# Kernel optimization log

Hardware: AMD Instinct MI355X
Metric: run time of the kernel (lower is better)

The kernel has to match this reference:

```python
import jax, jax.numpy as jnp
import numpy as np

B, T, D, H = 4, 1024, 1024, 16
DS, DC, EXP = 16, 4, 2
DI = EXP * D            # 2048 inner SSM dim
DTR = D // 16           # 64 dt rank
K = max(1, int(0.2 * T))  # top-k tokens routed to attention
HD = D // H


def setup_inputs() -> dict:
    key = jax.random.key(0)
    ks = jax.random.split(key, 12)
    s = 0.02
    w = lambda k, shp: jax.random.normal(k, shp, jnp.float32) * s
    return {
        "x": jax.random.normal(ks[0], (B, T, D), jnp.float32),
        "ln_gamma": jnp.ones((D,), jnp.float32),
        "ln_beta": jnp.zeros((D,), jnp.float32),
        "Wr1": w(ks[1], (D, D // 4)), "br1": jnp.zeros((D // 4,), jnp.float32),
        "Wr2": w(ks[2], (D // 4, 1)), "br2": jnp.zeros((1,), jnp.float32),
        "Wqkv": w(ks[3], (D, 3 * D)), "bqkv": jnp.zeros((3 * D,), jnp.float32),
        "Wo": w(ks[4], (D, D)), "bo": jnp.zeros((D,), jnp.float32),
        "W_in": w(ks[5], (D, 2 * DI)),
        "conv_w": w(ks[6], (DI, DC)), "conv_b": jnp.zeros((DI,), jnp.float32),
        "W_xproj": w(ks[7], (DI, DTR + 2 * DS)),
        "W_dt": w(ks[8], (DTR, DI)), "b_dt": jnp.zeros((DI,), jnp.float32),
        "A_log": jnp.log(jnp.broadcast_to(jnp.arange(1, DS + 1, dtype=jnp.float32), (DI, DS))),
        "Dskip": jnp.ones((DI,), jnp.float32),
        "W_out": w(ks[9], (DI, D)),
    }


def _layernorm(x, g, b):
    mu = x.mean(-1, keepdims=True)
    v = ((x - mu) ** 2).mean(-1, keepdims=True)
    return (x - mu) * jax.lax.rsqrt(v + 1e-5) * g + b


def _attn(tok, Wqkv, bqkv, Wo, bo):
    # full MHA over the k selected tokens only: tok (B,K,D)
    qkv = tok @ Wqkv + bqkv
    q, k_, v = jnp.split(qkv, 3, axis=-1)
    q = q.reshape(B, K, H, HD).transpose(0, 2, 1, 3)   # bhkd
    k_ = k_.reshape(B, K, H, HD).transpose(0, 2, 1, 3)
    v = v.reshape(B, K, H, HD).transpose(0, 2, 1, 3)
    scores = jnp.einsum('bhqd,bhkd->bhqk', q, k_) / jnp.sqrt(jnp.float32(HD))
    p = jax.nn.softmax(scores, axis=-1)
    o = jnp.einsum('bhqk,bhkd->bhqd', p, v)
    o = o.transpose(0, 2, 1, 3).reshape(B, K, D)
    return o @ Wo + bo


def _ssm(xn, W_in, conv_w, conv_b, W_xproj, W_dt, b_dt, A_log, Dskip, W_out):
    # Mamba-style selective SSM over all tokens
    u, z = jnp.split(xn @ W_in, 2, axis=-1)            # (B,T,DI) each
    up = jnp.pad(u, ((0, 0), (DC - 1, 0), (0, 0)))      # causal depthwise conv
    uc = sum(up[:, j:j + T, :] * conv_w[:, j] for j in range(DC)) + conv_b
    u = jax.nn.silu(uc)
    proj = u @ W_xproj                                  # (B,T,DTR+2*DS)
    dt = jax.nn.softplus(proj[..., :DTR] @ W_dt + b_dt)  # (B,T,DI)
    Bm = proj[..., DTR:DTR + DS]                        # (B,T,DS)
    Cm = proj[..., DTR + DS:]                           # (B,T,DS)
    A = -jnp.exp(A_log)                                 # (DI,DS)
    dA = jnp.exp(dt[..., None] * A)                     # (B,T,DI,DS)
    dBu = dt[..., None] * Bm[:, :, None, :] * u[..., None]

    def step(h, inp):
        dA_t, dBu_t, C_t = inp
        h = dA_t * h + dBu_t                            # (B,DI,DS)
        y = (h * C_t[:, None, :]).sum(-1)               # (B,DI)
        return h, y

    h0 = jnp.zeros((B, DI, DS), dA.dtype)
    _, ys = jax.lax.scan(step, h0, (dA.transpose(1, 0, 2, 3),
                                    dBu.transpose(1, 0, 2, 3),
                                    Cm.transpose(1, 0, 2)))
    y = ys.transpose(1, 0, 2) + u * Dskip               # (B,T,DI)
    y = y * jax.nn.silu(z)
    return y @ W_out


def reference(x, ln_gamma, ln_beta, Wr1, br1, Wr2, br2, Wqkv, bqkv, Wo, bo,
              W_in, conv_w, conv_b, W_xproj, W_dt, b_dt, A_log, Dskip, W_out):
    xn = _layernorm(x, ln_gamma, ln_beta)
    scores = (jax.nn.relu(xn @ Wr1 + br1) @ Wr2 + br2)[..., 0]   # (B,T)
    _, idx = jax.lax.top_k(scores, K)                            # (B,K)
    bidx = jnp.arange(B)[:, None]
    mask = jnp.zeros((B, T), bool).at[bidx, idx].set(True)
    delta_ssm = _ssm(xn, W_in, conv_w, conv_b, W_xproj, W_dt, b_dt, A_log, Dskip, W_out)
    tok = xn[bidx, idx]                                          # gather (B,K,D)
    delta_tok = _attn(tok, Wqkv, bqkv, Wo, bo)
    delta_attn = jnp.zeros_like(xn).at[bidx, idx].set(delta_tok)  # scatter back
    delta = jnp.where(mask[..., None], delta_attn, delta_ssm)
    return x + delta
```

## Files before the change

### kernel.cpp

```cpp
#include <hip/hip_runtime.h>
#include <hip/hip_bf16.h>
#include <math.h>

#define BB   4
#define TT   1024
#define DD   1024
#define HH   16
#define DII  2048
#define DSS  16
#define DCC  4
#define KK   204
#define HDD  64
#define DTRR 64
#define NCH  32
#define LCH  32
#define KSPL 8
#define XPN  96
#define PRJ  128
#define RZ   8
#define RKC  3072

typedef short bf16x8 __attribute__((ext_vector_type(8)));
typedef short bf16x4v __attribute__((ext_vector_type(4)));
typedef float f32x4 __attribute__((ext_vector_type(4)));

#define GLDS16(g, l) __builtin_amdgcn_global_load_lds(                        \
    (const __attribute__((address_space(1))) void*)(g),                       \
    (__attribute__((address_space(3))) void*)(l), 16, 0, 0)

__device__ __forceinline__ ushort f2bu(float v) {
  __hip_bfloat16 h = __float2bfloat16(v);
  return __builtin_bit_cast(ushort, h);
}
__device__ __forceinline__ float b2f(ushort u) {
  __hip_bfloat16 h = __builtin_bit_cast(__hip_bfloat16, u);
  return __bfloat162float(h);
}

__device__ __forceinline__ float wave_sum(float v) {
#pragma unroll
  for (int o = 32; o > 0; o >>= 1) v += __shfl_xor(v, o, 64);
  return v;
}
__device__ __forceinline__ float block_sum256(float v, volatile float* sh) {
  v = wave_sum(v);
  if ((threadIdx.x & 63) == 0) sh[threadIdx.x >> 6] = v;
  __syncthreads();
  float r = sh[0] + sh[1] + sh[2] + sh[3];
  __syncthreads();
  return r;
}

__global__ __launch_bounds__(256) void layernorm_kernel(
    const float* __restrict__ x, const float* __restrict__ g,
    const float* __restrict__ be, ushort* __restrict__ xcat) {
  __shared__ float sh[4];
  int row = blockIdx.x;
  const float* xr = x + (size_t)row * DD;
  float v[4];
  float s = 0.f;
#pragma unroll
  for (int i = 0; i < 4; i++) { v[i] = xr[threadIdx.x + 256 * i]; s += v[i]; }
  float mean = block_sum256(s, sh) * (1.f / DD);
  float q = 0.f;
#pragma unroll
  for (int i = 0; i < 4; i++) { float d = v[i] - mean; q += d * d; }
  float var = block_sum256(q, sh) * (1.f / DD);
  float rstd = rsqrtf(var + 1e-5f);
  ushort* xc = xcat + (size_t)row * RKC;
#pragma unroll
  for (int i = 0; i < 4; i++) {
    int c = threadIdx.x + 256 * i;
    float o = (v[i] - mean) * rstd * g[c] + be[c];
    ushort hi = f2bu(o);
    float lo = o - b2f(hi);
    xc[c] = hi;
    xc[1024 + c] = hi;
    xc[2048 + c] = f2bu(lo);
  }
}

__device__ __forceinline__ void tile_transpose(
    const float* W, int rows, int cols, ushort* WT, int bx, int by,
    float tile[32][33]) {
  int c0 = bx * 32, r0 = by * 32;
  int tx = threadIdx.x & 31, ty = threadIdx.x >> 5;
#pragma unroll
  for (int i = 0; i < 32; i += 8)
    tile[ty + i][tx] = W[(size_t)(r0 + ty + i) * cols + c0 + tx];
  __syncthreads();
#pragma unroll
  for (int i = 0; i < 32; i += 8)
    WT[(size_t)(c0 + ty + i) * rows + r0 + tx] = f2bu(tile[tx][ty + i]);
}

__global__ __launch_bounds__(256) void transpose_all(
    const float* __restrict__ W_in, const float* __restrict__ W_out,
    const float* __restrict__ Wqkv, const float* __restrict__ Wo,
    const float* __restrict__ W_dt, const float* __restrict__ W_xproj,
    ushort* __restrict__ WinT, ushort* __restrict__ WoutT,
    ushort* __restrict__ WqkvT, ushort* __restrict__ WoT,
    ushort* __restrict__ WdtT, ushort* __restrict__ WxprojT) {
  __shared__ float tile[32][33];
  int lin = blockIdx.x;
  if (lin < 4096) {
    tile_transpose(W_in, 1024, 4096, WinT, lin % 128, lin / 128, tile);
  } else if ((lin -= 4096) < 2048) {
    tile_transpose(W_out, 2048, 1024, WoutT, lin % 32, lin / 32, tile);
  } else if ((lin -= 2048) < 3072) {
    tile_transpose(Wqkv, 1024, 3072, WqkvT, lin % 96, lin / 96, tile);
  } else if ((lin -= 3072) < 1024) {
    tile_transpose(Wo, 1024, 1024, WoT, lin % 32, lin / 32, tile);
  } else if ((lin -= 1024) < 128) {
    tile_transpose(W_dt, 64, 2048, WdtT, lin % 64, lin / 64, tile);
  } else {
    lin -= 128;
    tile_transpose(W_xproj, 2048, 96, WxprojT, lin % 3, lin / 3, tile);
  }
}

__global__ __launch_bounds__(256) void transpose_hilo(
    const float* __restrict__ W, ushort* __restrict__ WT) {
  __shared__ float tile[32][33];
  int c0 = blockIdx.x * 32, r0 = blockIdx.y * 32;
  int tx = threadIdx.x & 31, ty = threadIdx.x >> 5;
#pragma unroll
  for (int i = 0; i < 32; i += 8)
    tile[ty + i][tx] = W[(size_t)(r0 + ty + i) * 256 + c0 + tx];
  __syncthreads();
#pragma unroll
  for (int i = 0; i < 32; i += 8) {
    float v = tile[tx][ty + i];
    ushort hi = f2bu(v);
    float lo = v - b2f(hi);
    size_t base = (size_t)(c0 + ty + i) * RKC;
    WT[base + r0 + tx] = hi;
    WT[base + 1024 + r0 + tx] = f2bu(lo);
    WT[base + 2048 + r0 + tx] = hi;
  }
}

__global__ __launch_bounds__(512) void gemm_bf16_256(
    const ushort* __restrict__ A, int lda,
    const ushort* __restrict__ BT, int ldbt,
    void* __restrict__ Cv, int ldc, int K,
    const float* __restrict__ bias, const float* __restrict__ addmat,
    int outBf16) {
  __shared__ ushort Alds[256 * 64];
  __shared__ ushort Blds[256 * 64];
  int t = threadIdx.x;
  int wv = t >> 6, lane = t & 63;
  int wvm = wv >> 2, wvn = wv & 3;
  int nwg = gridDim.x * gridDim.y;
  int lin = blockIdx.y * gridDim.x + blockIdx.x;
  int swz = (lin & 7) * (nwg >> 3) + (lin >> 3);
  int bx = swz % gridDim.x, by = swz / gridDim.x;
  int row0 = by * 256, col0 = bx * 256;
  f32x4 acc[8][4] = {};

  const ushort* Ap[4];
  const ushort* Bp[4];
  ushort* Alb[4];
  ushort* Blb[4];
#pragma unroll
  for (int j = 0; j < 4; j++) {
    int c = j * 512 + t;
    int r = c >> 3;
    int kc = (((c & 7) ^ (r & 7)) * 8);
    Ap[j] = A + (size_t)(row0 + r) * lda + kc;
    Bp[j] = BT + (size_t)(col0 + r) * ldbt + kc;
    int cst = j * 512 + wv * 64;
    Alb[j] = Alds + (size_t)cst * 8;
    Blb[j] = Blds + (size_t)cst * 8;
  }
  int frow = lane & 15, fk = (lane >> 4) * 8;

  for (int k0 = 0; k0 < K; k0 += 64) {
#pragma unroll
    for (int j = 0; j < 4; j++) {
      GLDS16(Ap[j] + k0, Alb[j]);
      GLDS16(Bp[j] + k0, Blb[j]);
    }
    __syncthreads();
#pragma unroll
    for (int ks = 0; ks < 2; ks++) {
      bf16x8 af[8], bfv[4];
#pragma unroll
      for (int m = 0; m < 8; m++) {
        int row = wvm * 128 + m * 16 + frow;
        af[m] = *(const bf16x8*)&Alds[row * 64 +
                                      ((ks * 32 + fk) ^ ((row & 7) * 8))];
      }
#pragma unroll
      for (int n = 0; n < 4; n++) {
        int row = wvn * 64 + n * 16 + frow;
        bfv[n] = *(const bf16x8*)&Blds[row * 64 +
                                       ((ks * 32 + fk) ^ ((row & 7) * 8))];
      }
#pragma unroll
      for (int m = 0; m < 8; m++)
#pragma unroll
        for (int n = 0; n < 4; n++)
          acc[m][n] = __builtin_amdgcn_mfma_f32_16x16x32_bf16(af[m], bfv[n],
                                                              acc[m][n], 0, 0, 0);
    }
    __syncthreads();
  }
  int rbase = row0 + wvm * 128 + (lane >> 4) * 4;
  int cbase = col0 + wvn * 64 + (lane & 15);
  if (outBf16) {
    ushort* myL = Alds + wv * 1088;
    ushort* C16 = (ushort*)Cv;
    for (int m = 0; m < 8; m++) {
      __syncthreads();
#pragma unroll
      for (int n = 0; n < 4; n++) {
        int cc = cbase + n * 16;
        float bi = bias ? bias[cc] : 0.f;
#pragma unroll
        for (int i = 0; i < 4; i++)
          myL[((lane >> 4) * 4 + i) * 68 + (lane & 15) + n * 16] =
              f2bu(acc[m][n][i] + bi);
      }
      __syncthreads();
      int rr = lane >> 2, cg = lane & 3;
      bf16x8 v0 = *(const bf16x8*)&myL[rr * 68 + cg * 16];
      bf16x8 v1 = *(const bf16x8*)&myL[rr * 68 + cg * 16 + 8];
      size_t grow = (size_t)(row0 + wvm * 128 + m * 16 + rr) * ldc +
                    col0 + wvn * 64 + cg * 16;
      *(bf16x8*)&C16[grow] = v0;
      *(bf16x8*)&C16[grow + 8] = v1;
    }
  } else {
    float* C = (float*)Cv;
#pragma unroll
    for (int n = 0; n < 4; n++) {
      int cc = cbase + n * 16;
      float bi = bias ? bias[cc] : 0.f;
#pragma unroll
      for (int m = 0; m < 8; m++) {
#pragma unroll
        for (int i = 0; i < 4; i++) {
          size_t r = rbase + m * 16 + i;
          float v = acc[m][n][i] + bi;
          if (addmat) v += addmat[r * ldc + cc];
          C[r * ldc + cc] = v;
        }
      }
    }
  }
}

__global__ __launch_bounds__(512) void gemm_bf16_128x8(
    const ushort* __restrict__ A, int lda,
    const ushort* __restrict__ BT, int ldbt,
    void* __restrict__ Cv, int ldc, int K,
    const float* __restrict__ bias, const float* __restrict__ addmat,
    int act, int outBf16) {
  __shared__ ushort Alds[128 * 64];
  __shared__ ushort Blds[128 * 64];
  int t = threadIdx.x;
  int wv = t >> 6, lane = t & 63;
  int wvm = wv >> 1, wvn = wv & 1;
  int nwg = gridDim.x * gridDim.y;
  int lin = blockIdx.y * gridDim.x + blockIdx.x;
  int swz = (lin & 7) * (nwg >> 3) + (lin >> 3);
  int bx = swz % gridDim.x, by = swz / gridDim.x;
  int row0 = by * 128, col0 = bx * 128;
  f32x4 acc[2][4] = {};

  const ushort* Ap[2];
  const ushort* Bp[2];
  ushort* Alb[2];
  ushort* Blb[2];
#pragma unroll
  for (int j = 0; j < 2; j++) {
    int c = j * 512 + t;
    int r = c >> 3;
    int kc = (((c & 7) ^ (r & 7)) * 8);
    Ap[j] = A + (size_t)(row0 + r) * lda + kc;
    Bp[j] = BT + (size_t)(col0 + r) * ldbt + kc;
    int cst = j * 512 + wv * 64;
    Alb[j] = Alds + (size_t)cst * 8;
    Blb[j] = Blds + (size_t)cst * 8;
  }
  int frow = lane & 15, fk = (lane >> 4) * 8;

  for (int k0 = 0; k0 < K; k0 += 64) {
#pragma unroll
    for (int j = 0; j < 2; j++) {
      GLDS16(Ap[j] + k0, Alb[j]);
      GLDS16(Bp[j] + k0, Blb[j]);
    }
    __syncthreads();
#pragma unroll
    for (int ks = 0; ks < 2; ks++) {
      bf16x8 af[2], bfv[4];
#pragma unroll
      for (int m = 0; m < 2; m++) {
        int row = wvm * 32 + m * 16 + frow;
        af[m] = *(const bf16x8*)&Alds[row * 64 +
                                      ((ks * 32 + fk) ^ ((row & 7) * 8))];
      }
#pragma unroll
      for (int n = 0; n < 4; n++) {
        int row = wvn * 64 + n * 16 + frow;
        bfv[n] = *(const bf16x8*)&Blds[row * 64 +
                                       ((ks * 32 + fk) ^ ((row & 7) * 8))];
      }
#pragma unroll
      for (int m = 0; m < 2; m++)
#pragma unroll
        for (int n = 0; n < 4; n++)
          acc[m][n] = __builtin_amdgcn_mfma_f32_16x16x32_bf16(af[m], bfv[n],
                                                              acc[m][n], 0, 0, 0);
    }
    __syncthreads();
  }
  int rbase = row0 + wvm * 32 + (lane >> 4) * 4;
  int cbase = col0 + wvn * 64 + (lane & 15);
#pragma unroll
  for (int n = 0; n < 4; n++) {
    int cc = cbase + n * 16;
    float bi = bias ? bias[cc] : 0.f;
#pragma unroll
    for (int m = 0; m < 2; m++) {
#pragma unroll
      for (int i = 0; i < 4; i++) {
        size_t r = rbase + m * 16 + i;
        float v = acc[m][n][i] + bi;
        if (act == 2) v = (v > 20.f) ? v : log1pf(__expf(v));
        if (outBf16) {
          ((ushort*)Cv)[r * ldc + cc] = f2bu(v);
        } else {
          if (addmat) v += addmat[r * ldc + cc];
          ((float*)Cv)[r * ldc + cc] = v;
        }
      }
    }
  }
}

__global__ __launch_bounds__(512) void gemm_bf16_128x8_splitk(
    const ushort* __restrict__ A, int lda,
    const ushort* __restrict__ BT, int ldbt,
    float* __restrict__ partial, int ldc, int Ktot, size_t zstride) {
  __shared__ ushort Alds[128 * 64];
  __shared__ ushort Blds[128 * 64];
  int t = threadIdx.x;
  int wv = t >> 6, lane = t & 63;
  int wvm = wv >> 1, wvn = wv & 1;
  int nwg = gridDim.x * gridDim.y;
  int lin = blockIdx.y * gridDim.x + blockIdx.x;
  int swz = (lin & 7) * (nwg >> 3) + (lin >> 3);
  int bx = swz % gridDim.x, by = swz / gridDim.x;
  int row0 = by * 128, col0 = bx * 128;
  int kchunk = Ktot / gridDim.z;
  int kbeg = blockIdx.z * kchunk, kend = kbeg + kchunk;
  f32x4 acc[2][4] = {};

  const ushort* Ap[2];
  const ushort* Bp[2];
  ushort* Alb[2];
  ushort* Blb[2];
#pragma unroll
  for (int j = 0; j < 2; j++) {
    int c = j * 512 + t;
    int r = c >> 3;
    int kc = (((c & 7) ^ (r & 7)) * 8);
    Ap[j] = A + (size_t)(row0 + r) * lda + kc;
    Bp[j] = BT + (size_t)(col0 + r) * ldbt + kc;
    int cst = j * 512 + wv * 64;
    Alb[j] = Alds + (size_t)cst * 8;
    Blb[j] = Blds + (size_t)cst * 8;
  }
  int frow = lane & 15, fk = (lane >> 4) * 8;

  for (int k0 = kbeg; k0 < kend; k0 += 64) {
#pragma unroll
    for (int j = 0; j < 2; j++) {
      GLDS16(Ap[j] + k0, Alb[j]);
      GLDS16(Bp[j] + k0, Blb[j]);
    }
    __syncthreads();
#pragma unroll
    for (int ks = 0; ks < 2; ks++) {
      bf16x8 af[2], bfv[4];
#pragma unroll
      for (int m = 0; m < 2; m++) {
        int row = wvm * 32 + m * 16 + frow;
        af[m] = *(const bf16x8*)&Alds[row * 64 +
                                      ((ks * 32 + fk) ^ ((row & 7) * 8))];
      }
#pragma unroll
      for (int n = 0; n < 4; n++) {
        int row = wvn * 64 + n * 16 + frow;
        bfv[n] = *(const bf16x8*)&Blds[row * 64 +
                                       ((ks * 32 + fk) ^ ((row & 7) * 8))];
      }
#pragma unroll
      for (int m = 0; m < 2; m++)
#pragma unroll
        for (int n = 0; n < 4; n++)
          acc[m][n] = __builtin_amdgcn_mfma_f32_16x16x32_bf16(af[m], bfv[n],
                                                              acc[m][n], 0, 0, 0);
    }
    __syncthreads();
  }
  float* P = partial + (size_t)blockIdx.z * zstride;
  int rbase = row0 + wvm * 32 + (lane >> 4) * 4;
  int cbase = col0 + wvn * 64 + (lane & 15);
#pragma unroll
  for (int n = 0; n < 4; n++) {
    int cc = cbase + n * 16;
#pragma unroll
    for (int m = 0; m < 2; m++)
#pragma unroll
      for (int i = 0; i < 4; i++)
        P[(size_t)(rbase + m * 16 + i) * ldc + cc] = acc[m][n][i];
  }
}

__global__ __launch_bounds__(256) void router_score_reduce(
    const float* __restrict__ rpart, const float* __restrict__ br1,
    const float* __restrict__ Wr2, const float* __restrict__ br2,
    float* __restrict__ scores, size_t zstride) {
  __shared__ float sh[4];
  int row = blockIdx.x, c = threadIdx.x;
  size_t idx = (size_t)row * 256 + c;
  float s = 0.f;
#pragma unroll
  for (int z = 0; z < RZ; z++) s += rpart[z * zstride + idx];
  s = fmaxf(s + br1[c], 0.f);
  float tot = block_sum256(s * Wr2[c], sh);
  if (c == 0) scores[row] = tot + br2[0];
}

__global__ __launch_bounds__(256) void gemm_bf16_mfma(
    const ushort* __restrict__ A, int lda,
    const ushort* __restrict__ BT, int ldbt,
    float* __restrict__ C, int ldc,
    int M, int N, int K, const float* __restrict__ bias,
    const float* __restrict__ addmat, const int* __restrict__ rowmap) {
  __shared__ ushort Alds[128 * 32];
  __shared__ ushort Blds[128 * 32];
  int t = threadIdx.x;
  int wv = t >> 6;
  int lane = t & 63;
  int nwg = gridDim.x * gridDim.y;
  int lin = blockIdx.y * gridDim.x + blockIdx.x;
  int swz = (lin & 7) * (nwg >> 3) + (lin >> 3);
  int bx = swz % gridDim.x, by = swz / gridDim.x;
  int row0 = by * 128, col0 = bx * 128;
  int wr = (wv >> 1) * 64, wc = (wv & 1) * 64;
  f32x4 acc[4][4] = {};

  int srow = t >> 2;
  int sk = (((t & 3) ^ (srow & 3)) * 8);
  int ar0 = row0 + srow;       if (ar0 >= M) ar0 = M - 1;
  int ar1 = row0 + 64 + srow;  if (ar1 >= M) ar1 = M - 1;
  int br0 = col0 + srow;       if (br0 >= N) br0 = N - 1;
  int br1 = col0 + 64 + srow;  if (br1 >= N) br1 = N - 1;
  const ushort* Ag0 = A + (size_t)ar0 * lda + sk;
  const ushort* Ag1 = A + (size_t)ar1 * lda + sk;
  const ushort* Bg0 = BT + (size_t)br0 * ldbt + sk;
  const ushort* Bg1 = BT + (size_t)br1 * ldbt + sk;
  ushort* Al = Alds + wv * 512;
  ushort* Bl = Blds + wv * 512;

  int frow = lane & 15;
  int fk = (lane >> 4) * 8;

  for (int k0 = 0; k0 < K; k0 += 32) {
    GLDS16(Ag0 + k0, Al);
    GLDS16(Ag1 + k0, Al + 2048);
    GLDS16(Bg0 + k0, Bl);
    GLDS16(Bg1 + k0, Bl + 2048);
    __syncthreads();
    bf16x8 af[4], bfv[4];
#pragma unroll
    for (int m = 0; m < 4; m++) {
      int row = wr + m * 16 + frow;
      af[m] = *(const bf16x8*)&Alds[row * 32 + (fk ^ ((row & 3) * 8))];
    }
#pragma unroll
    for (int n = 0; n < 4; n++) {
      int row = wc + n * 16 + frow;
      bfv[n] = *(const bf16x8*)&Blds[row * 32 + (fk ^ ((row & 3) * 8))];
    }
#pragma unroll
    for (int m = 0; m < 4; m++)
#pragma unroll
      for (int n = 0; n < 4; n++)
        acc[m][n] = __builtin_amdgcn_mfma_f32_16x16x32_bf16(af[m], bfv[n],
                                                            acc[m][n], 0, 0, 0);
    __syncthreads();
  }
  int rbase = row0 + wr + (lane >> 4) * 4;
  int cbase = col0 + wc + (lane & 15);
#pragma unroll
  for (int n = 0; n < 4; n++) {
    int ccol = cbase + n * 16;
    if (ccol >= N) continue;
    float bi = bias ? bias[ccol] : 0.f;
#pragma unroll
    for (int m = 0; m < 4; m++) {
      int r0_ = rbase + m * 16;
#pragma unroll
      for (int i = 0; i < 4; i++) {
        int r = r0_ + i;
        if (r < M) {
          size_t orow = r;
          if (rowmap) orow = (size_t)((r / KK) * TT + rowmap[r]);
          float v = acc[m][n][i] + bi;
          if (addmat) v += addmat[orow * ldc + ccol];
          C[orow * ldc + ccol] = v;
        }
      }
    }
  }
}

__global__ __launch_bounds__(1024) void topk_kernel(
    const float* __restrict__ scores, int* __restrict__ idx) {
  __shared__ float s[1024];
  __shared__ int si[1024];
  int b = blockIdx.x, t = threadIdx.x;
  s[t] = scores[b * TT + t];
  si[t] = t;
  __syncthreads();
  for (int k = 2; k <= 1024; k <<= 1) {
    for (int j = k >> 1; j > 0; j >>= 1) {
      int partner = t ^ j;
      if (partner > t) {
        bool dirDesc = ((t & k) == 0);
        float s1 = s[t], s2 = s[partner];
        int i1 = si[t], i2 = si[partner];
        bool firstGreater = (s1 > s2) || (s1 == s2 && i1 < i2);
        bool doSwap = dirDesc ? !firstGreater : firstGreater;
        if (doSwap) { s[t] = s2; s[partner] = s1; si[t] = i2; si[partner] = i1; }
      }
      __syncthreads();
    }
  }
  if (t < KK) idx[b * KK + t] = si[t];
}

__global__ __launch_bounds__(256) void splitk_reduce_dual(
    const float* __restrict__ partial, float* __restrict__ C,
    __hip_bfloat16* __restrict__ Cb, int MN) {
  int i = blockIdx.x * 256 + threadIdx.x;
  if (i >= MN) return;
  float s = 0.f;
#pragma unroll
  for (int k = 0; k < KSPL; k++) s += partial[(size_t)k * MN + i];
  C[i] = s;
  Cb[i] = __float2bfloat16(s);
}

__global__ __launch_bounds__(256) void conv_silu_kernel(
    const ushort* __restrict__ uz, const float* __restrict__ conv_w,
    const float* __restrict__ conv_b, ushort* __restrict__ ub16) {
  size_t gid4 = ((size_t)blockIdx.x * 256 + threadIdx.x) * 4;
  int c = gid4 % DII;
  size_t bt = gid4 / DII;
  int t = bt % TT;
  int b = bt / TT;
  f32x4 cw[4];
#pragma unroll
  for (int ci = 0; ci < 4; ci++) cw[ci] = *(const f32x4*)&conv_w[(c + ci) * DCC];
  f32x4 sum = *(const f32x4*)&conv_b[c];
#pragma unroll
  for (int j = 0; j < DCC; j++) {
    int tt = t - (DCC - 1) + j;
    if (tt >= 0) {
      bf16x4v uv = *(const bf16x4v*)&uz[((size_t)(b * TT + tt)) * (2 * DII) + c];
#pragma unroll
      for (int ci = 0; ci < 4; ci++) sum[ci] += b2f((ushort)uv[ci]) * cw[ci][j];
    }
  }
  bf16x4v rb;
#pragma unroll
  for (int ci = 0; ci < 4; ci++)
    rb[ci] = (short)f2bu(sum[ci] / (1.f + __expf(-sum[ci])));
  *(bf16x4v*)&ub16[gid4] = rb;
}

__global__ __launch_bounds__(256) void ssm_phase1(
    const ushort* __restrict__ dt, const float* __restrict__ proj,
    const ushort* __restrict__ u, const float* __restrict__ A_log,
    float* __restrict__ hloc, float* __restrict__ Pprod) {
  int gid = blockIdx.x * 256 + threadIdx.x;
  int half = gid & 1;
  int cc = gid >> 1;
  int di = cc % DII;
  int rem = cc / DII;
  int chunk = rem % NCH;
  int b = rem / NCH;
  float a[8], h[8], P[8];
#pragma unroll
  for (int i = 0; i < 2; i++) {
    f32x4 al = *(const f32x4*)&A_log[di * DSS + half * 8 + i * 4];
#pragma unroll
    for (int j = 0; j < 4; j++) a[i * 4 + j] = -__expf(al[j]);
  }
#pragma unroll
  for (int s = 0; s < 8; s++) { h[s] = 0.f; P[s] = 1.f; }
  int t0 = chunk * LCH;
  for (int lt = 0; lt < LCH; lt++) {
    size_t bt = (size_t)(b * TT + t0 + lt);
    float dtv = b2f(dt[bt * DII + di]);
    float uv = b2f(u[bt * DII + di]);
    const float* pr = proj + bt * PRJ + DTRR + half * 8;
    float dtu = dtv * uv;
#pragma unroll
    for (int s = 0; s < 8; s++) {
      float dA = __expf(dtv * a[s]);
      h[s] = dA * h[s] + dtu * pr[s];
      P[s] *= dA;
    }
  }
#pragma unroll
  for (int i = 0; i < 2; i++) {
    *(f32x4*)&hloc[(size_t)cc * 16 + half * 8 + i * 4] = *(f32x4*)&h[i * 4];
    *(f32x4*)&Pprod[(size_t)cc * 16 + half * 8 + i * 4] = *(f32x4*)&P[i * 4];
  }
}

__global__ __launch_bounds__(256) void ssm_phase2(
    const float* __restrict__ hloc, const float* __restrict__ Pprod,
    float* __restrict__ hin) {
  int gid = blockIdx.x * 256 + threadIdx.x;
  int s_di = gid % (DII * 16);
  int b = gid / (DII * 16);
  float run = 0.f;
#pragma unroll
  for (int c = 0; c < NCH; c++) {
    size_t off = ((size_t)(b * NCH + c) * DII) * 16 + s_di;
    hin[off] = run;
    run = Pprod[off] * run + hloc[off];
  }
}

__global__ __launch_bounds__(256) void ssm_phase3(
    const ushort* __restrict__ dt, const float* __restrict__ proj,
    const ushort* __restrict__ u, const ushort* __restrict__ uz,
    const float* __restrict__ A_log, const float* __restrict__ Dskip,
    const float* __restrict__ hin, __hip_bfloat16* __restrict__ y) {
  int gid = blockIdx.x * 256 + threadIdx.x;
  int half = gid & 1;
  int cc = gid >> 1;
  int di = cc % DII;
  int rem = cc / DII;
  int chunk = rem % NCH;
  int b = rem / NCH;
  float a[8], h[8];
#pragma unroll
  for (int i = 0; i < 2; i++) {
    f32x4 al = *(const f32x4*)&A_log[di * DSS + half * 8 + i * 4];
    f32x4 hl = *(const f32x4*)&hin[(size_t)cc * 16 + half * 8 + i * 4];
#pragma unroll
    for (int j = 0; j < 4; j++) { a[i * 4 + j] = -__expf(al[j]); h[i * 4 + j] = hl[j]; }
  }
  float dsk = Dskip[di];
  int t0 = chunk * LCH;
  for (int lt = 0; lt < LCH; lt++) {
    size_t bt = (size_t)(b * TT + t0 + lt);
    float dtv = b2f(dt[bt * DII + di]);
    float uv = b2f(u[bt * DII + di]);
    const float* prB = proj + bt * PRJ + DTRR + half * 8;
    const float* prC = prB + DSS;
    float dtu = dtv * uv;
    float yp = 0.f;
#pragma unroll
    for (int s = 0; s < 8; s++) {
      float dA = __expf(dtv * a[s]);
      h[s] = dA * h[s] + dtu * prB[s];
      yp += h[s] * prC[s];
    }
    yp += __shfl_xor(yp, 1, 64);
    if (half == 0) {
      float zv = b2f(uz[bt * (2 * DII) + DII + di]);
      float sz = zv / (1.f + __expf(-zv));
      y[bt * DII + di] = __float2bfloat16((yp + uv * dsk) * sz);
    }
  }
}

__global__ __launch_bounds__(256) void gather_tok(
    const ushort* __restrict__ xcat, const int* __restrict__ idx,
    ushort* __restrict__ tok) {
  int r = blockIdx.x;
  int b = r / KK;
  int tsel = idx[r];
  const ushort* src = xcat + (size_t)(b * TT + tsel) * RKC;
  ushort* dst = tok + (size_t)r * DD;
#pragma unroll
  for (int j = 0; j < 4; j++) dst[threadIdx.x + 256 * j] = src[threadIdx.x + 256 * j];
}

#define KP 72
#define VP 232
__global__ __launch_bounds__(832) void attn_mfma_kernel(
    const float* __restrict__ qkv, __hip_bfloat16* __restrict__ attn_o) {
  __shared__ ushort Klds[208 * KP];
  __shared__ ushort VTlds[64 * VP];
  __shared__ ushort Plds[13 * 16 * VP];
  int bh = blockIdx.x;
  int h = bh % HH, b = bh / HH;
  int t = threadIdx.x;
  const float* base = qkv + (size_t)(b * KK) * 3072 + h * 64;

  for (int i = t; i < 208 * 64; i += 832) {
    int r = i >> 6, d = i & 63;
    float v = (r < KK) ? base[(size_t)r * 3072 + 1024 + d] : 0.f;
    Klds[r * KP + d] = f2bu(v);
  }
  for (int i = t; i < 208 * 64; i += 832) {
    int r = i >> 6, d = i & 63;
    float v = (r < KK) ? base[(size_t)r * 3072 + 2048 + d] : 0.f;
    VTlds[d * VP + r] = f2bu(v);
  }
  for (int i = t; i < 64 * (VP - 208); i += 832) {
    int d = i / (VP - 208), k = 208 + i % (VP - 208);
    VTlds[d * VP + k] = 0;
  }

  int wv = t >> 6, lane = t & 63;
  int q0 = wv * 16;
  int qrow = q0 + (lane & 15);
  if (qrow > KK - 1) qrow = KK - 1;
  const float* qptr = base + (size_t)qrow * 3072 + ((lane >> 4) * 8);
  bf16x8 qf[2];
#pragma unroll
  for (int ks = 0; ks < 2; ks++) {
    f32x4 lo = *(const f32x4*)(qptr + ks * 32);
    f32x4 hi = *(const f32x4*)(qptr + ks * 32 + 4);
#pragma unroll
    for (int j = 0; j < 4; j++) {
      qf[ks][j] = (short)f2bu(lo[j] * 0.125f);
      qf[ks][j + 4] = (short)f2bu(hi[j] * 0.125f);
    }
  }
  ushort* myP = Plds + wv * 16 * VP;
  for (int i = lane; i < 16 * (VP - 208); i += 64) {
    int r = i / (VP - 208), k = 208 + i % (VP - 208);
    myP[r * VP + k] = 0;
  }
  __syncthreads();

  f32x4 sacc[13] = {};
#pragma unroll
  for (int nt = 0; nt < 13; nt++) {
#pragma unroll
    for (int ks = 0; ks < 2; ks++) {
      bf16x8 kf = *(const bf16x8*)&Klds[(nt * 16 + (lane & 15)) * KP +
                                        ks * 32 + (lane >> 4) * 8];
      sacc[nt] = __builtin_amdgcn_mfma_f32_16x16x32_bf16(qf[ks], kf, sacc[nt], 0, 0, 0);
    }
  }
  if ((lane & 15) >= 12) {
#pragma unroll
    for (int i = 0; i < 4; i++) sacc[12][i] = -1e30f;
  }
  float m4[4], l4[4];
#pragma unroll
  for (int i = 0; i < 4; i++) {
    float m = sacc[0][i];
#pragma unroll
    for (int nt = 1; nt < 13; nt++) m = fmaxf(m, sacc[nt][i]);
    m = fmaxf(m, __shfl_xor(m, 1, 64));
    m = fmaxf(m, __shfl_xor(m, 2, 64));
    m = fmaxf(m, __shfl_xor(m, 4, 64));
    m = fmaxf(m, __shfl_xor(m, 8, 64));
    m4[i] = m;
  }
#pragma unroll
  for (int i = 0; i < 4; i++) {
    float ls = 0.f;
    int prow = (lane >> 4) * 4 + i;
#pragma unroll
    for (int nt = 0; nt < 13; nt++) {
      float e = __expf(sacc[nt][i] - m4[i]);
      ls += e;
      myP[prow * VP + nt * 16 + (lane & 15)] = f2bu(e);
    }
    ls += __shfl_xor(ls, 1, 64);
    ls += __shfl_xor(ls, 2, 64);
    ls += __shfl_xor(ls, 4, 64);
    ls += __shfl_xor(ls, 8, 64);
    l4[i] = ls;
  }
  f32x4 oacc[4] = {};
#pragma unroll
  for (int dt = 0; dt < 4; dt++) {
#pragma unroll
    for (int ks = 0; ks < 7; ks++) {
      bf16x8 pf = *(const bf16x8*)&myP[(lane & 15) * VP + ks * 32 + (lane >> 4) * 8];
      bf16x8 vf = *(const bf16x8*)&VTlds[(dt * 16 + (lane & 15)) * VP +
                                         ks * 32 + (lane >> 4) * 8];
      oacc[dt] = __builtin_amdgcn_mfma_f32_16x16x32_bf16(pf, vf, oacc[dt], 0, 0, 0);
    }
  }
#pragma unroll
  for (int i = 0; i < 4; i++) {
    int row = q0 + (lane >> 4) * 4 + i;
    if (row >= KK) continue;
    float inv = 1.f / l4[i];
#pragma unroll
    for (int dt = 0; dt < 4; dt++) {
      int col = dt * 16 + (lane & 15);
      attn_o[((size_t)(b * KK + row)) * DD + h * 64 + col] =
          __float2bfloat16(oacc[dt][i] * inv);
    }
  }
}

extern "C" void kernel_launch(void* const* d_in, const int* in_sizes, int n_in,
                              void* d_out, int out_size, void* d_ws, size_t ws_size,
                              hipStream_t stream) {
  const float* x = (const float*)d_in[0];
  const float* ln_g = (const float*)d_in[1];
  const float* ln_b = (const float*)d_in[2];
  const float* Wr1 = (const float*)d_in[3];
  const float* br1 = (const float*)d_in[4];
  const float* Wr2 = (const float*)d_in[5];
  const float* br2 = (const float*)d_in[6];
  const float* Wqkv = (const float*)d_in[7];
  const float* bqkv = (const float*)d_in[8];
  const float* Wo = (const float*)d_in[9];
  const float* bo = (const float*)d_in[10];
  const float* W_in = (const float*)d_in[11];
  const float* conv_w = (const float*)d_in[12];
  const float* conv_b = (const float*)d_in[13];
  const float* W_xproj = (const float*)d_in[14];
  const float* W_dt = (const float*)d_in[15];
  const float* b_dt = (const float*)d_in[16];
  const float* A_log = (const float*)d_in[17];
  const float* Dskip = (const float*)d_in[18];
  const float* W_out = (const float*)d_in[19];
  float* out = (float*)d_out;

  float* w = (float*)d_ws;
  size_t o = 0;
  float* scores = w + o; o += (size_t)BB * TT;
  int* idxb = (int*)(w + o); o += 1024;
  ushort* uzb16 = (ushort*)(w + o); o += (size_t)BB * TT * 2 * DII / 2;
  float* projb = w + o;  o += (size_t)BB * TT * PRJ;
  float* qkvb = w + o;   o += (size_t)BB * KK * 3 * DD;
  float* hloc = w + o;   o += (size_t)BB * NCH * DII * 16;
  float* Pprod = w + o;  o += (size_t)BB * NCH * DII * 16;
  float* hin = w + o;    o += (size_t)BB * NCH * DII * 16;
  ushort* xcat = (ushort*)(w + o);                  o += (size_t)BB * TT * RKC / 2;
  __hip_bfloat16* yb16 = (__hip_bfloat16*)(w + o);  o += (size_t)BB * TT * DII / 2;
  ushort* ub16 = (ushort*)(w + o);                  o += (size_t)BB * TT * DII / 2;
  ushort* dtb16 = (ushort*)(w + o);                 o += (size_t)BB * TT * DII / 2;
  ushort* tokb = (ushort*)(w + o);                  o += (size_t)BB * KK * DD / 2 + 8;
  __hip_bfloat16* attno = (__hip_bfloat16*)(w + o); o += (size_t)BB * KK * DD / 2 + 8;
  __hip_bfloat16* projb16 = (__hip_bfloat16*)(w + o); o += (size_t)BB * TT * PRJ / 2 + 8;
  ushort* Wr1cat = (ushort*)(w + o);                o += (size_t)256 * RKC / 2;
  ushort* WinT = (ushort*)(w + o);                  o += (size_t)(2 * DII) * DD / 2;
  ushort* WoutT = (ushort*)(w + o);                 o += (size_t)DD * DII / 2;
  ushort* WqkvT = (ushort*)(w + o);                 o += (size_t)(3 * DD) * DD / 2;
  ushort* WoT = (ushort*)(w + o);                   o += (size_t)DD * DD / 2;
  ushort* WdtT = (ushort*)(w + o);                  o += (size_t)DII * DTRR / 2;
  ushort* WxprojT = (ushort*)(w + o);               o += (size_t)PRJ * DII / 2;
  float* rpart = (float*)uzb16;
  float* xpart = hloc;
  const size_t RZSTR = (size_t)BB * TT * 256;
  const size_t XZSTR = (size_t)BB * TT * PRJ;

  layernorm_kernel<<<BB * TT, 256, 0, stream>>>(x, ln_g, ln_b, xcat);
  transpose_all<<<10560, 256, 0, stream>>>(W_in, W_out, Wqkv, Wo, W_dt, W_xproj,
                                           WinT, WoutT, WqkvT, WoT, WdtT, WxprojT);
  transpose_hilo<<<dim3(256 / 32, DD / 32), 256, 0, stream>>>(Wr1, Wr1cat);
  gemm_bf16_128x8_splitk<<<dim3(256 / 128, BB * TT / 128, RZ), 512, 0, stream>>>(
      xcat, RKC, Wr1cat, RKC, rpart, 256, RKC, RZSTR);
  router_score_reduce<<<BB * TT, 256, 0, stream>>>(rpart, br1, Wr2, br2, scores,
                                                   RZSTR);
  topk_kernel<<<BB, 1024, 0, stream>>>(scores, idxb);
  gemm_bf16_256<<<dim3(2 * DII / 256, BB * TT / 256), 512, 0, stream>>>(
      xcat, RKC, WinT, DD, uzb16, 2 * DII, DD, nullptr, nullptr, 1);
  conv_silu_kernel<<<(BB * TT * DII) / 1024, 256, 0, stream>>>(uzb16, conv_w,
                                                               conv_b, ub16);
  gemm_bf16_128x8_splitk<<<dim3(PRJ / 128, BB * TT / 128, KSPL), 512, 0, stream>>>(
      ub16, DII, WxprojT, DII, xpart, PRJ, DII, XZSTR);
  splitk_reduce_dual<<<(int)((XZSTR + 255) / 256), 256, 0, stream>>>(
      xpart, projb, projb16, (int)XZSTR);
  gemm_bf16_128x8<<<dim3(DII / 128, BB * TT / 128), 512, 0, stream>>>(
      (const ushort*)projb16, PRJ, WdtT, DTRR, dtb16, DII, DTRR,
      b_dt, nullptr, 2, 1);
  ssm_phase1<<<(BB * NCH * DII * 2) / 256, 256, 0, stream>>>(dtb16, projb, ub16,
                                                             A_log, hloc, Pprod);
  ssm_phase2<<<(BB * DII * 16) / 256, 256, 0, stream>>>(hloc, Pprod, hin);
  ssm_phase3<<<(BB * NCH * DII * 2) / 256, 256, 0, stream>>>(dtb16, projb, ub16,
                                                             uzb16, A_log, Dskip,
                                                             hin, yb16);
  gemm_bf16_128x8<<<dim3(DD / 128, BB * TT / 128), 512, 0, stream>>>(
      (const ushort*)yb16, DII, WoutT, DII, out, DD, DII,
      nullptr, x, 0, 0);
  gather_tok<<<BB * KK, 256, 0, stream>>>(xcat, idxb, tokb);
  gemm_bf16_mfma<<<dim3(3 * DD / 128, (BB * KK + 127) / 128), 256, 0, stream>>>(
      tokb, DD, WqkvT, DD, qkvb, 3 * DD,
      BB * KK, 3 * DD, DD, bqkv, nullptr, nullptr);
  attn_mfma_kernel<<<BB * HH, 832, 0, stream>>>(qkvb, attno);
  gemm_bf16_mfma<<<dim3(DD / 128, (BB * KK + 127) / 128), 256, 0, stream>>>(
      (const ushort*)attno, DD, WoT, DD, out, DD,
      BB * KK, DD, DD, bo, x, idxb);
}
```

Baseline: 431.2 us.

## Route attention GEMMs through the tuned kernel with bf16 QKV and split-K Wo

Replaces the generic 128x128 MFMA GEMM for the QKV and output projections with the existing gemm_bf16_128x8 kernels, padding the selected-token rows to 896. The QKV output is now stored in bf16, which halves its traffic and removes the fp32-to-bf16 conversion inside attention. The 1/sqrt(d) scale moves from Q onto the scores. The Wo projection is split along K into four partials, and a new reduce kernel sums them, adds bias and residual, and scatters rows to the output. This trades an extra partial buffer and reduce pass for better parallelism on the small-M GEMM.

After: 381.3 us. 1.13x faster.

```diff
diff --git a/kernel.cpp b/kernel.cpp
--- a/kernel.cpp
+++ b/kernel.cpp
@@ -19,6 +19,8 @@
 #define PRJ  128
 #define RZ   8
 #define RKC  3072
+#define MPAD 896
+#define WOZ  4
 
 typedef short bf16x8 __attribute__((ext_vector_type(8)));
 typedef short bf16x4v __attribute__((ext_vector_type(4)));
@@ -436,89 +438,26 @@
   if (c == 0) scores[row] = tot + br2[0];
 }
 
-__global__ __launch_bounds__(256) void gemm_bf16_mfma(
-    const ushort* __restrict__ A, int lda,
-    const ushort* __restrict__ BT, int ldbt,
-    float* __restrict__ C, int ldc,
-    int M, int N, int K, const float* __restrict__ bias,
-    const float* __restrict__ addmat, const int* __restrict__ rowmap) {
-  __shared__ ushort Alds[128 * 32];
-  __shared__ ushort Blds[128 * 32];
-  int t = threadIdx.x;
-  int wv = t >> 6;
-  int lane = t & 63;
-  int nwg = gridDim.x * gridDim.y;
-  int lin = blockIdx.y * gridDim.x + blockIdx.x;
-  int swz = (lin & 7) * (nwg >> 3) + (lin >> 3);
-  int bx = swz % gridDim.x, by = swz / gridDim.x;
-  int row0 = by * 128, col0 = bx * 128;
-  int wr = (wv >> 1) * 64, wc = (wv & 1) * 64;
-  f32x4 acc[4][4] = {};
-
-  int srow = t >> 2;
-  int sk = (((t & 3) ^ (srow & 3)) * 8);
-  int ar0 = row0 + srow;       if (ar0 >= M) ar0 = M - 1;
-  int ar1 = row0 + 64 + srow;  if (ar1 >= M) ar1 = M - 1;
-  int br0 = col0 + srow;       if (br0 >= N) br0 = N - 1;
-  int br1 = col0 + 64 + srow;  if (br1 >= N) br1 = N - 1;
-  const ushort* Ag0 = A + (size_t)ar0 * lda + sk;
-  const ushort* Ag1 = A + (size_t)ar1 * lda + sk;
-  const ushort* Bg0 = BT + (size_t)br0 * ldbt + sk;
-  const ushort* Bg1 = BT + (size_t)br1 * ldbt + sk;
-  ushort* Al = Alds + wv * 512;
-  ushort* Bl = Blds + wv * 512;
-
-  int frow = lane & 15;
-  int fk = (lane >> 4) * 8;
-
-  for (int k0 = 0; k0 < K; k0 += 32) {
-    GLDS16(Ag0 + k0, Al);
-    GLDS16(Ag1 + k0, Al + 2048);
-    GLDS16(Bg0 + k0, Bl);
-    GLDS16(Bg1 + k0, Bl + 2048);
-    __syncthreads();
-    bf16x8 af[4], bfv[4];
-#pragma unroll
-    for (int m = 0; m < 4; m++) {
-      int row = wr + m * 16 + frow;
-      af[m] = *(const bf16x8*)&Alds[row * 32 + (fk ^ ((row & 3) * 8))];
-    }
-#pragma unroll
-    for (int n = 0; n < 4; n++) {
-      int row = wc + n * 16 + frow;
-      bfv[n] = *(const bf16x8*)&Blds[row * 32 + (fk ^ ((row & 3) * 8))];
-    }
-#pragma unroll
-    for (int m = 0; m < 4; m++)
-#pragma unroll
-      for (int n = 0; n < 4; n++)
-        acc[m][n] = __builtin_amdgcn_mfma_f32_16x16x32_bf16(af[m], bfv[n],
-                                                            acc[m][n], 0, 0, 0);
-    __syncthreads();
-  }
-  int rbase = row0 + wr + (lane >> 4) * 4;
-  int cbase = col0 + wc + (lane & 15);
-#pragma unroll
-  for (int n = 0; n < 4; n++) {
-    int ccol = cbase + n * 16;
-    if (ccol >= N) continue;
-    float bi = bias ? bias[ccol] : 0.f;
-#pragma unroll
-    for (int m = 0; m < 4; m++) {
-      int r0_ = rbase + m * 16;
-#pragma unroll
-      for (int i = 0; i < 4; i++) {
-        int r = r0_ + i;
-        if (r < M) {
-          size_t orow = r;
-          if (rowmap) orow = (size_t)((r / KK) * TT + rowmap[r]);
-          float v = acc[m][n][i] + bi;
-          if (addmat) v += addmat[orow * ldc + ccol];
-          C[orow * ldc + ccol] = v;
-        }
-      }
-    }
-  }
+__global__ __launch_bounds__(256) void wo_scatter_reduce(
+    const float* __restrict__ wpart, const float* __restrict__ x,
+    const float* __restrict__ bo, const int* __restrict__ idx,
+    float* __restrict__ out, size_t zstride) {
+  int r = blockIdx.x;
+  int b = r / KK;
+  size_t orow = (size_t)(b * TT + idx[r]) * DD;
+  int c4 = threadIdx.x * 4;
+  f32x4 s = *(const f32x4*)&wpart[(size_t)r * DD + c4];
+#pragma unroll
+  for (int z = 1; z < WOZ; z++) {
+    f32x4 p = *(const f32x4*)&wpart[z * zstride + (size_t)r * DD + c4];
+#pragma unroll
+    for (int j = 0; j < 4; j++) s[j] += p[j];
+  }
+  f32x4 xv = *(const f32x4*)&x[orow + c4];
+  f32x4 bv = *(const f32x4*)&bo[c4];
+#pragma unroll
+  for (int j = 0; j < 4; j++) s[j] += xv[j] + bv[j];
+  *(f32x4*)&out[orow + c4] = s;
 }
 
 __global__ __launch_bounds__(1024) void topk_kernel(
@@ -702,24 +641,22 @@
 #define KP 72
 #define VP 232
 __global__ __launch_bounds__(832) void attn_mfma_kernel(
-    const float* __restrict__ qkv, __hip_bfloat16* __restrict__ attn_o) {
+    const ushort* __restrict__ qkv, ushort* __restrict__ attn_o) {
   __shared__ ushort Klds[208 * KP];
   __shared__ ushort VTlds[64 * VP];
   __shared__ ushort Plds[13 * 16 * VP];
   int bh = blockIdx.x;
   int h = bh % HH, b = bh / HH;
   int t = threadIdx.x;
-  const float* base = qkv + (size_t)(b * KK) * 3072 + h * 64;
+  const ushort* base = qkv + (size_t)(b * KK) * 3072 + h * 64;
 
   for (int i = t; i < 208 * 64; i += 832) {
     int r = i >> 6, d = i & 63;
-    float v = (r < KK) ? base[(size_t)r * 3072 + 1024 + d] : 0.f;
-    Klds[r * KP + d] = f2bu(v);
+    Klds[r * KP + d] = (r < KK) ? base[(size_t)r * 3072 + 1024 + d] : (ushort)0;
   }
   for (int i = t; i < 208 * 64; i += 832) {
     int r = i >> 6, d = i & 63;
-    float v = (r < KK) ? base[(size_t)r * 3072 + 2048 + d] : 0.f;
-    VTlds[d * VP + r] = f2bu(v);
+    VTlds[d * VP + r] = (r < KK) ? base[(size_t)r * 3072 + 2048 + d] : (ushort)0;
   }
   for (int i = t; i < 64 * (VP - 208); i += 832) {
     int d = i / (VP - 208), k = 208 + i % (VP - 208);
@@ -730,18 +667,10 @@
   int q0 = wv * 16;
   int qrow = q0 + (lane & 15);
   if (qrow > KK - 1) qrow = KK - 1;
-  const float* qptr = base + (size_t)qrow * 3072 + ((lane >> 4) * 8);
+  const ushort* qptr = base + (size_t)qrow * 3072 + ((lane >> 4) * 8);
   bf16x8 qf[2];
 #pragma unroll
-  for (int ks = 0; ks < 2; ks++) {
-    f32x4 lo = *(const f32x4*)(qptr + ks * 32);
-    f32x4 hi = *(const f32x4*)(qptr + ks * 32 + 4);
-#pragma unroll
-    for (int j = 0; j < 4; j++) {
-      qf[ks][j] = (short)f2bu(lo[j] * 0.125f);
-      qf[ks][j + 4] = (short)f2bu(hi[j] * 0.125f);
-    }
-  }
+  for (int ks = 0; ks < 2; ks++) qf[ks] = *(const bf16x8*)(qptr + ks * 32);
   ushort* myP = Plds + wv * 16 * VP;
   for (int i = lane; i < 16 * (VP - 208); i += 64) {
     int r = i / (VP - 208), k = 208 + i % (VP - 208);
@@ -758,6 +687,8 @@
                                         ks * 32 + (lane >> 4) * 8];
       sacc[nt] = __builtin_amdgcn_mfma_f32_16x16x32_bf16(qf[ks], kf, sacc[nt], 0, 0, 0);
     }
+#pragma unroll
+    for (int i = 0; i < 4; i++) sacc[nt][i] *= 0.125f;
   }
   if ((lane & 15) >= 12) {
 #pragma unroll
@@ -811,7 +742,7 @@
     for (int dt = 0; dt < 4; dt++) {
       int col = dt * 16 + (lane & 15);
       attn_o[((size_t)(b * KK + row)) * DD + h * 64 + col] =
-          __float2bfloat16(oacc[dt][i] * inv);
+          f2bu(oacc[dt][i] * inv);
     }
   }
 }
@@ -847,7 +778,7 @@
   int* idxb = (int*)(w + o); o += 1024;
   ushort* uzb16 = (ushort*)(w + o); o += (size_t)BB * TT * 2 * DII / 2;
   float* projb = w + o;  o += (size_t)BB * TT * PRJ;
-  float* qkvb = w + o;   o += (size_t)BB * KK * 3 * DD;
+  ushort* qkvb16 = (ushort*)(w + o); o += (size_t)MPAD * 3 * DD / 2 + 8;
   float* hloc = w + o;   o += (size_t)BB * NCH * DII * 16;
   float* Pprod = w + o;  o += (size_t)BB * NCH * DII * 16;
   float* hin = w + o;    o += (size_t)BB * NCH * DII * 16;
@@ -855,8 +786,8 @@
   __hip_bfloat16* yb16 = (__hip_bfloat16*)(w + o);  o += (size_t)BB * TT * DII / 2;
   ushort* ub16 = (ushort*)(w + o);                  o += (size_t)BB * TT * DII / 2;
   ushort* dtb16 = (ushort*)(w + o);                 o += (size_t)BB * TT * DII / 2;
-  ushort* tokb = (ushort*)(w + o);                  o += (size_t)BB * KK * DD / 2 + 8;
-  __hip_bfloat16* attno = (__hip_bfloat16*)(w + o); o += (size_t)BB * KK * DD / 2 + 8;
+  ushort* tokb = (ushort*)(w + o);                  o += (size_t)MPAD * DD / 2 + 8;
+  ushort* attno = (ushort*)(w + o);                 o += (size_t)MPAD * DD / 2 + 8;
   __hip_bfloat16* projb16 = (__hip_bfloat16*)(w + o); o += (size_t)BB * TT * PRJ / 2 + 8;
   ushort* Wr1cat = (ushort*)(w + o);                o += (size_t)256 * RKC / 2;
   ushort* WinT = (ushort*)(w + o);                  o += (size_t)(2 * DII) * DD / 2;
@@ -867,8 +798,10 @@
   ushort* WxprojT = (ushort*)(w + o);               o += (size_t)PRJ * DII / 2;
   float* rpart = (float*)uzb16;
   float* xpart = hloc;
+  float* wpart = hloc;
   const size_t RZSTR = (size_t)BB * TT * 256;
   const size_t XZSTR = (size_t)BB * TT * PRJ;
+  const size_t WZSTR = (size_t)MPAD * DD;
 
   layernorm_kernel<<<BB * TT, 256, 0, stream>>>(x, ln_g, ln_b, xcat);
   transpose_all<<<10560, 256, 0, stream>>>(W_in, W_out, Wqkv, Wo, W_dt, W_xproj,
@@ -900,11 +833,10 @@
       (const ushort*)yb16, DII, WoutT, DII, out, DD, DII,
       nullptr, x, 0, 0);
   gather_tok<<<BB * KK, 256, 0, stream>>>(xcat, idxb, tokb);
-  gemm_bf16_mfma<<<dim3(3 * DD / 128, (BB * KK + 127) / 128), 256, 0, stream>>>(
-      tokb, DD, WqkvT, DD, qkvb, 3 * DD,
-      BB * KK, 3 * DD, DD, bqkv, nullptr, nullptr);
-  attn_mfma_kernel<<<BB * HH, 832, 0, stream>>>(qkvb, attno);
-  gemm_bf16_mfma<<<dim3(DD / 128, (BB * KK + 127) / 128), 256, 0, stream>>>(
-      (const ushort*)attno, DD, WoT, DD, out, DD,
-      BB * KK, DD, DD, bo, x, idxb);
-}
+  gemm_bf16_128x8<<<dim3(3 * DD / 128, MPAD / 128), 512, 0, stream>>>(
+      tokb, DD, WqkvT, DD, qkvb16, 3 * DD, DD, bqkv, nullptr, 0, 1);
+  attn_mfma_kernel<<<BB * HH, 832, 0, stream>>>(qkvb16, attno);
+  gemm_bf16_128x8_splitk<<<dim3(DD / 128, MPAD / 128, WOZ), 512, 0, stream>>>(
+      attno, DD, WoT, DD, wpart, DD, DD, WZSTR);
+  wo_scatter_reduce<<<BB * KK, 256, 0, stream>>>(wpart, x, bo, idxb, out, WZSTR);
+}
```
